# Kernel optimization log

Hardware: AMD Instinct MI355X
Metric: run time of the kernel (lower is better)

## Reference

```python
import jax, jax.numpy as jnp
import numpy as np

COULOMB_CONSTANT = 14.399645351950548  # eV * Angstrom
ENERGY_SCALE = 1.0
NOISE = 1e-8  # numerical_noise added to pairwise distances
B, N, D, U, E = 64, 512, 128, 64, 7


def tanhshrink(x):
    return x - jnp.tanh(x)


def chi_mlp(h, W1, b1, W2, b2, W3, b3):
    # MLP(dims=[D, U, U, 1], activation=Tanhshrink, activate_last=True)
    h = tanhshrink(h @ W1 + b1)
    h = tanhshrink(h @ W2 + b2)
    h = tanhshrink(h @ W3 + b3)
    return h  # [..., 1]


def setup_inputs() -> dict:
    key = jax.random.key(0)
    ks = jax.random.split(key, 8)
    return {
        "pos": jax.random.normal(ks[0], (B, N, 3), dtype=jnp.float32) * 3.0,
        "node_feats": jax.random.normal(ks[1], (B, N, D), dtype=jnp.float32),
        "node_type": jax.random.randint(ks[2], (B, N), 0, E),
        "total_charge": jax.random.normal(ks[3], (B,), dtype=jnp.float32),
        "hardness": jnp.ones((E,), dtype=jnp.float32),   # hardness_readout Parameter
        "sigma": jnp.ones((E,), dtype=jnp.float32),      # sigma Parameter (is_sigma_train)
        "W1": jax.random.normal(ks[4], (D, U), dtype=jnp.float32) / np.float32(np.sqrt(D)),
        "b1": jnp.zeros((U,), dtype=jnp.float32),
        "W2": jax.random.normal(ks[5], (U, U), dtype=jnp.float32) / np.float32(np.sqrt(U)),
        "b2": jnp.zeros((U,), dtype=jnp.float32),
        "W3": jax.random.normal(ks[6], (U, 1), dtype=jnp.float32) / np.float32(np.sqrt(U)),
        "b3": jnp.zeros((1,), dtype=jnp.float32),
    }


def reference(pos, node_feats, node_type, total_charge, hardness, sigma,
              W1, b1, W2, b2, W3, b3):
    k = jnp.float32(COULOMB_CONSTANT / ENERGY_SCALE)
    chi = chi_mlp(node_feats, W1, b1, W2, b2, W3, b3)[..., 0]          # [B, N]
    hard = hardness[node_type]                                          # [B, N]
    sig = sigma[node_type]                                              # [B, N]

    # Pairwise distances (per graph, dense O(N^2))
    diff = pos[:, :, None, :] - pos[:, None, :, :]                      # [B, N, N, 3]
    bond_dist = jnp.sqrt(jnp.sum(diff * diff, axis=-1)) + NOISE         # [B, N, N]
    gamma_ij = jnp.sqrt(sig[:, :, None] ** 2 + sig[:, None, :] ** 2)    # [B, N, N]

    a = k * jax.lax.erf(bond_dist / (jnp.sqrt(jnp.float32(2.0)) * gamma_ij)) / bond_dist

    # Diagonal self term: hardness_i + k / (sqrt(pi) * gamma_ii), gamma_ii = sqrt(2)*sigma_i
    gamma_ii = jnp.sqrt(jnp.float32(2.0)) * sig                         # [B, N]
    diag = hard + k / (jnp.sqrt(jnp.float32(np.pi)) * gamma_ii)         # [B, N]
    idx = jnp.arange(N)
    A = a.at[:, idx, idx].add(diag)                                     # [B, N, N]

    # Bordered system enforcing total charge constraint
    Bm = jnp.ones((B, N + 1, N + 1), dtype=pos.dtype)
    Bm = Bm.at[:, :N, :N].set(A)
    Bm = Bm.at[:, N, N].set(0.0)
    rhs = jnp.concatenate([-chi, total_charge[:, None]], axis=1)        # [B, N+1]

    x = jnp.linalg.solve(Bm, rhs[..., None])[..., 0]                    # [B, N+1]
    charges = x[:, :N]
    return charges, A
```

## Files before the change

kernel.cpp:

```cpp
#include <hip/hip_runtime.h>
#include <math.h>

constexpr int BB = 64, NN = 512, DD = 128, UU = 64;
constexpr float KCOUL = 14.399645351950548f;
constexpr float NOISEF = 1e-8f;
#define M_PIF 3.14159265358979323846f

typedef __attribute__((ext_vector_type(8))) short bfrag;
typedef __attribute__((ext_vector_type(4))) float ffrag;

__device__ __forceinline__ unsigned short f2bf(float f) {
  unsigned int u = __float_as_uint(f);
  u += 0x7fffu + ((u >> 16) & 1u);
  return (unsigned short)(u >> 16);
}
__device__ __forceinline__ float bf2f(unsigned short h) {
  return __uint_as_float((unsigned int)h << 16);
}
__device__ __forceinline__ float fast_erf(float x) {
  float t2 = x * x;
  float small_v = 1.1283791671f * x *
      fmaf(t2, fmaf(t2, fmaf(t2, fmaf(t2, 4.6296296e-3f, -2.3809524e-2f),
                             0.1f), -0.33333333f), 1.0f);
  float t = __builtin_amdgcn_rcpf(fmaf(0.3275911f, x, 1.0f));
  float p = fmaf(fmaf(fmaf(fmaf(1.061405429f, t, -1.453152027f),
                           t, 1.421413741f), t, -0.284496736f), t, 0.254829592f);
  float big_v = fmaf(-p * t, __expf(-t2), 1.0f);
  return x < 0.5f ? small_v : big_v;
}
__device__ __forceinline__ float fast_tanh(float x) {
  float ax = fabsf(x);
  float e = __expf(2.0f * ax);
  float t = 1.0f - 2.0f * __builtin_amdgcn_rcpf(e + 1.0f);
  return __builtin_copysignf(t, x);
}

__global__ __launch_bounds__(256) void chi_kernel(
    const float* __restrict__ feats, const float* __restrict__ W1,
    const float* __restrict__ b1, const float* __restrict__ W2,
    const float* __restrict__ b2, const float* __restrict__ W3,
    const float* __restrict__ b3, float* __restrict__ chi)
{
  int wave = threadIdx.x >> 6, lane = threadIdx.x & 63;
  int row0 = __builtin_amdgcn_readfirstlane((blockIdx.x * 4 + wave) * 4);
  const float* f = feats + (size_t)row0 * DD;
  __shared__ float sh[4][4][UU];

  float a0 = b1[lane], a1 = a0, a2 = a0, a3 = a0;
  #pragma unroll 8
  for (int d = 0; d < DD; ++d) {
    float wv = W1[d * UU + lane];
    a0 = fmaf(f[d],          wv, a0);
    a1 = fmaf(f[DD + d],     wv, a1);
    a2 = fmaf(f[2 * DD + d], wv, a2);
    a3 = fmaf(f[3 * DD + d], wv, a3);
  }
  sh[wave][0][lane] = a0 - fast_tanh(a0);
  sh[wave][1][lane] = a1 - fast_tanh(a1);
  sh[wave][2][lane] = a2 - fast_tanh(a2);
  sh[wave][3][lane] = a3 - fast_tanh(a3);
  __builtin_amdgcn_s_waitcnt(0);
  float c0 = b2[lane], c1 = c0, c2 = c0, c3 = c0;
  #pragma unroll 8
  for (int u = 0; u < UU; ++u) {
    float wv = W2[u * UU + lane];
    c0 = fmaf(sh[wave][0][u], wv, c0);
    c1 = fmaf(sh[wave][1][u], wv, c1);
    c2 = fmaf(sh[wave][2][u], wv, c2);
    c3 = fmaf(sh[wave][3][u], wv, c3);
  }
  float w3 = W3[lane];
  float p0 = (c0 - fast_tanh(c0)) * w3;
  float p1 = (c1 - fast_tanh(c1)) * w3;
  float p2 = (c2 - fast_tanh(c2)) * w3;
  float p3 = (c3 - fast_tanh(c3)) * w3;
  #pragma unroll
  for (int off = 32; off; off >>= 1) {
    p0 += __shfl_down(p0, off, 64);
    p1 += __shfl_down(p1, off, 64);
    p2 += __shfl_down(p2, off, 64);
    p3 += __shfl_down(p3, off, 64);
  }
  if (lane == 0) {
    float bb = b3[0];
    float z0 = p0 + bb, z1 = p1 + bb, z2v = p2 + bb, z3 = p3 + bb;
    chi[row0]     = z0 - fast_tanh(z0);
    chi[row0 + 1] = z1 - fast_tanh(z1);
    chi[row0 + 2] = z2v - fast_tanh(z2v);
    chi[row0 + 3] = z3 - fast_tanh(z3);
  }
}

__global__ __launch_bounds__(256) void build_A_kernel(
    const float* __restrict__ pos, const int* __restrict__ ntype,
    const float* __restrict__ hardness, const float* __restrict__ sigma,
    float* __restrict__ Aout, unsigned short* __restrict__ Abf)
{
  int b = blockIdx.y;
  int r0 = blockIdx.x * 16;
  __shared__ float px[NN], py[NN], pz[NN], s2[NN], hd[NN];
  __shared__ unsigned short tile[16 * NN];
  for (int n = threadIdx.x; n < NN; n += 256) {
    const float* p = pos + ((size_t)b * NN + n) * 3;
    px[n] = p[0]; py[n] = p[1]; pz[n] = p[2];
    int ty = ntype[b * NN + n];
    float s = sigma[ty];
    s2[n] = s * s;
    hd[n] = hardness[ty];
  }
  __syncthreads();
  int c0 = (threadIdx.x & 127) << 2;
  int rsub = threadIdx.x >> 7;
  float* outB = Aout + (size_t)b * NN * NN;
  for (int k = 0; k < 8; ++k) {
    int i = r0 + (k << 1) + rsub;
    float pxi = px[i], pyi = py[i], pzi = pz[i], s2i = s2[i];
    float4 v;
    float* vp = &v.x;
    #pragma unroll
    for (int c = 0; c < 4; ++c) {
      int j = c0 + c;
      float dx = pxi - px[j], dy = pyi - py[j], dz = pzi - pz[j];
      float d = sqrtf(fmaf(dx, dx, fmaf(dy, dy, dz * dz))) + NOISEF;
      float arg = d * __builtin_amdgcn_rsqf(2.0f * (s2i + s2[j]));
      float val = KCOUL * fast_erf(arg) * __builtin_amdgcn_rcpf(d);
      if (j == i) val += hd[i] + KCOUL * __builtin_amdgcn_rsqf(2.0f * M_PIF * s2i);
      vp[c] = val;
    }
    *reinterpret_cast<float4*>(outB + (size_t)i * NN + c0) = v;
    if (Abf) {
      ushort4 wv;
      wv.x = f2bf(v.x); wv.y = f2bf(v.y); wv.z = f2bf(v.z); wv.w = f2bf(v.w);
      int loc = ((c0 >> 5) << 9) + (((c0 >> 3) & 3) << 7) + ((i & 15) << 3) + (c0 & 7);
      *reinterpret_cast<ushort4*>(tile + loc) = wv;
    }
  }
  if (Abf) {
    __syncthreads();
    const uint4* src = reinterpret_cast<const uint4*>(tile);
    uint4* dst = reinterpret_cast<uint4*>(Abf + (size_t)b * NN * NN +
                                          ((size_t)(r0 >> 4) << 13));
    #pragma unroll
    for (int k = 0; k < 4; ++k)
      dst[threadIdx.x + k * 256] = src[threadIdx.x + k * 256];
  }
}

__device__ __forceinline__ float4 blockReduce4(float4 v, float4* wred, int t) {
  #pragma unroll
  for (int off = 32; off; off >>= 1) {
    v.x += __shfl_down(v.x, off, 64);
    v.y += __shfl_down(v.y, off, 64);
    v.z += __shfl_down(v.z, off, 64);
    v.w += __shfl_down(v.w, off, 64);
  }
  __syncthreads();
  if ((t & 63) == 0) wred[t >> 6] = v;
  __syncthreads();
  float4 r = wred[0];
  #pragma unroll
  for (int k = 1; k < 16; ++k) {
    float4 u = wred[k];
    r.x += u.x; r.y += u.y; r.z += u.z; r.w += u.w;
  }
  return r;
}

__global__ __launch_bounds__(1024) void cg_kernel_bf(
    const unsigned short* __restrict__ Abf, const float* __restrict__ tq,
    float* __restrict__ qout )
{
  int b = blockIdx.x;
  const unsigned short* A = Abf + (size_t)b * NN * NN;
  int t = threadIdx.x;
  int lane = t & 63, w = t >> 6;
  constexpr int PAD = NN + 32;
  __shared__ float2 p01[NN], q01[NN], r01[NN], x01[NN], w01[NN];
  __shared__ __align__(16) unsigned short rsplit[4 * PAD];
  __shared__ float4 wred[16];

  float2 z2 = make_float2(0.f, 0.f);
  float2 rsq = z2;
  if (t < NN) {
    float c = qout[b * NN + t];
    float2 rv = make_float2(-c, 1.0f);
    r01[t] = rv; x01[t] = z2; p01[t] = z2; q01[t] = z2;
    unsigned short h0 = f2bf(rv.x), h1 = f2bf(rv.y);
    rsplit[t] = h0;            rsplit[PAD + t] = h1;
    rsplit[2 * PAD + t] = f2bf(rv.x - bf2f(h0));
    rsplit[3 * PAD + t] = f2bf(rv.y - bf2f(h1));
    rsq = make_float2(rv.x * rv.x, rv.y * rv.y);
  }
  float4 rr0 = blockReduce4(make_float4(rsq.x, rsq.y, 0.f, 0.f), wred, t);
  float tol0 = fmaxf(1e-4f * rr0.x, 1e-12f);
  float tol1 = fmaxf(1e-4f * rr0.y, 1e-12f);
  bool act0 = rr0.x > tol0, act1 = rr0.y > tol1;

  const int m  = lane & 15;
  const int qd = lane >> 4;
  const unsigned short* aw0 = A + ((size_t)(2 * w) << 13) + lane * 8;
  const unsigned short* aw1 = aw0 + 8192;
  const unsigned short* bhi = rsplit + (m & 1) * PAD;
  const unsigned short* blo = rsplit + 2 * PAD + (m & 1) * PAD;

  float muold0 = 1.f, muold1 = 1.f, alold0 = 1.f, alold1 = 1.f;
  for (int k = 0; k < 24 && (act0 || act1); ++k) {
    ffrag acc0 = {0.f, 0.f, 0.f, 0.f};
    ffrag acc1 = {0.f, 0.f, 0.f, 0.f};
    #pragma unroll 4
    for (int c = 0; c < 16; ++c) {
      int bo = c * 32 + qd * 8;
      bfrag bh = *reinterpret_cast<const bfrag*>(bhi + bo);
      bfrag bl = *reinterpret_cast<const bfrag*>(blo + bo);
      bfrag a0 = *reinterpret_cast<const bfrag*>(aw0 + c * 512);
      bfrag a1 = *reinterpret_cast<const bfrag*>(aw1 + c * 512);
      acc0 = __builtin_amdgcn_mfma_f32_16x16x32_bf16(a0, bh, acc0, 0, 0, 0);
      acc0 = __builtin_amdgcn_mfma_f32_16x16x32_bf16(a0, bl, acc0, 0, 0, 0);
      acc1 = __builtin_amdgcn_mfma_f32_16x16x32_bf16(a1, bh, acc1, 0, 0, 0);
      acc1 = __builtin_amdgcn_mfma_f32_16x16x32_bf16(a1, bl, acc1, 0, 0, 0);
    }
    if (m < 2) {
      int rbase = qd * 4;
      #pragma unroll
      for (int r = 0; r < 4; ++r) {
        reinterpret_cast<float*>(&w01[w * 32 + rbase + r])[m]      = acc0[r];
        reinterpret_cast<float*>(&w01[w * 32 + 16 + rbase + r])[m] = acc1[r];
      }
    }
    __syncthreads();

    float4 dp = make_float4(0.f, 0.f, 0.f, 0.f);
    if (t < NN) {
      float2 rv = r01[t], wv = w01[t];
      dp = make_float4(rv.x * rv.x, rv.x * wv.x, rv.y * rv.y, rv.y * wv.y);
    }
    float4 s = blockReduce4(dp, wred, t);
    if (act0 && s.x <= tol0) act0 = false;
    if (act1 && s.z <= tol1) act1 = false;
    if (!act0 && !act1) break;
    float be0 = 0.f, al0 = 0.f, be1 = 0.f, al1 = 0.f;
    if (act0) {
      be0 = k ? s.x / muold0 : 0.f;
      al0 = s.x / (s.y - be0 * s.x / alold0);
      muold0 = s.x; alold0 = al0;
    }
    if (act1) {
      be1 = k ? s.z / muold1 : 0.f;
      al1 = s.z / (s.w - be1 * s.z / alold1);
      muold1 = s.z; alold1 = al1;
    }

    if (t < NN) {
      float2 rv = r01[t], wv = w01[t], pv = p01[t], qv = q01[t], xv = x01[t];
      if (act0) {
        pv.x = fmaf(be0, pv.x, rv.x);
        qv.x = fmaf(be0, qv.x, wv.x);
        xv.x = fmaf(al0, pv.x, xv.x);
        rv.x = fmaf(-al0, qv.x, rv.x);
      }
      if (act1) {
        pv.y = fmaf(be1, pv.y, rv.y);
        qv.y = fmaf(be1, qv.y, wv.y);
        xv.y = fmaf(al1, pv.y, xv.y);
        rv.y = fmaf(-al1, qv.y, rv.y);
      }
      p01[t] = pv; q01[t] = qv; x01[t] = xv; r01[t] = rv;
      unsigned short h0 = f2bf(rv.x), h1 = f2bf(rv.y);
      rsplit[t] = h0;            rsplit[PAD + t] = h1;
      rsplit[2 * PAD + t] = f2bf(rv.x - bf2f(h0));
      rsplit[3 * PAD + t] = f2bf(rv.y - bf2f(h1));
    }
    __syncthreads();
  }

  float2 sv = z2;
  if (t < NN) sv = x01[t];
  float4 s = blockReduce4(make_float4(sv.x, sv.y, 0.f, 0.f), wred, t);
  float lam = (s.x - tq[b]) / s.y;
  if (t < NN) qout[b * NN + t] = x01[t].x - lam * x01[t].y;
}

__device__ __forceinline__ float2 blockReduce2(float2 v, float2* wred, int t) {
  #pragma unroll
  for (int off = 32; off; off >>= 1) {
    v.x += __shfl_down(v.x, off, 64);
    v.y += __shfl_down(v.y, off, 64);
  }
  __syncthreads();
  if ((t & 63) == 0) wred[t >> 6] = v;
  __syncthreads();
  float2 r = wred[0];
  #pragma unroll
  for (int k = 1; k < 16; ++k) { r.x += wred[k].x; r.y += wred[k].y; }
  return r;
}

__global__ __launch_bounds__(1024) void cg_kernel_f32(
    const float* __restrict__ Aall, const float* __restrict__ tq,
    float* __restrict__ qout)
{
  int b = blockIdx.x;
  const float* A = Aall + (size_t)b * NN * NN;
  int t = threadIdx.x;
  __shared__ float2 p01[NN], q01[NN], r01[NN], x01[NN];
  __shared__ float4 sacc0[8][128];
  __shared__ float4 sacc1[8][128];
  __shared__ float2 wred[16];

  float2 z2 = make_float2(0.f, 0.f);
  float2 rsq = z2;
  if (t < NN) {
    float b0 = -qout[b * NN + t];
    x01[t] = z2;
    r01[t] = make_float2(b0, 1.0f);
    p01[t] = make_float2(b0, 1.0f);
    rsq = make_float2(b0 * b0, 1.0f);
  }
  float2 rr = blockReduce2(rsq, wred, t);
  float tol0 = fmaxf(1e-4f * rr.x, 1e-12f);
  float tol1 = fmaxf(1e-4f * rr.y, 1e-12f);
  const int c4 = (t & 127) << 2;
  const int jr = t >> 7;
  for (int it = 0; it < 24; ++it) {
    bool act0 = rr.x > tol0, act1 = rr.y > tol1;
    if (!act0 && !act1) break;
    {
      const float* ap = A + (size_t)(jr * 64) * NN + c4;
      float4 a0 = make_float4(0.f, 0.f, 0.f, 0.f);
      float4 a1 = a0;
      #pragma unroll 8
      for (int mI = 0; mI < 64; ++mI) {
        float4 av = *reinterpret_cast<const float4*>(ap);
        ap += NN;
        float2 pj = p01[jr * 64 + mI];
        a0.x = fmaf(av.x, pj.x, a0.x); a0.y = fmaf(av.y, pj.x, a0.y);
        a0.z = fmaf(av.z, pj.x, a0.z); a0.w = fmaf(av.w, pj.x, a0.w);
        a1.x = fmaf(av.x, pj.y, a1.x); a1.y = fmaf(av.y, pj.y, a1.y);
        a1.z = fmaf(av.z, pj.y, a1.z); a1.w = fmaf(av.w, pj.y, a1.w);
      }
      sacc0[jr][t & 127] = a0;
      sacc1[jr][t & 127] = a1;
    }
    __syncthreads();
    float2 dv = z2;
    if (t < NN) {
      const float* f0 = reinterpret_cast<const float*>(sacc0);
      const float* f1 = reinterpret_cast<const float*>(sacc1);
      float s0 = 0.f, s1 = 0.f;
      #pragma unroll
      for (int g = 0; g < 8; ++g) { s0 += f0[g * 512 + t]; s1 += f1[g * 512 + t]; }
      q01[t] = make_float2(s0, s1);
      float2 pv = p01[t];
      dv.x = s0 * pv.x; dv.y = s1 * pv.y;
    }
    float2 pq = blockReduce2(dv, wred, t);
    float al0 = act0 ? rr.x / pq.x : 0.f;
    float al1 = act1 ? rr.y / pq.y : 0.f;
    float2 rn = z2;
    if (t < NN) {
      float2 xv = x01[t], rv = r01[t], pv = p01[t], qv = q01[t];
      xv.x = fmaf(al0, pv.x, xv.x);  xv.y = fmaf(al1, pv.y, xv.y);
      rv.x = fmaf(-al0, qv.x, rv.x); rv.y = fmaf(-al1, qv.y, rv.y);
      x01[t] = xv; r01[t] = rv;
      rn.x = rv.x * rv.x; rn.y = rv.y * rv.y;
    }
    float2 rrn = blockReduce2(rn, wred, t);
    float be0 = act0 ? rrn.x / rr.x : 0.f;
    float be1 = act1 ? rrn.y / rr.y : 0.f;
    if (t < NN) {
      float2 rv = r01[t], pv = p01[t];
      pv.x = fmaf(be0, pv.x, rv.x);
      pv.y = fmaf(be1, pv.y, rv.y);
      p01[t] = pv;
    }
    rr = rrn;
    __syncthreads();
  }
  float2 sv = z2;
  if (t < NN) sv = x01[t];
  float2 s = blockReduce2(sv, wred, t);
  float lam = (s.x - tq[b]) / s.y;
  if (t < NN) qout[b * NN + t] = x01[t].x - lam * x01[t].y;
}

extern "C" void kernel_launch(void* const* d_in, const int* in_sizes, int n_in,
                              void* d_out, int out_size, void* d_ws, size_t ws_size,
                              hipStream_t stream) {
  const float* pos      = (const float*)d_in[0];
  const float* feats    = (const float*)d_in[1];
  const int*   ntype    = (const int*)  d_in[2];
  const float* tq       = (const float*)d_in[3];
  const float* hardness = (const float*)d_in[4];
  const float* sigma    = (const float*)d_in[5];
  const float* W1 = (const float*)d_in[6];
  const float* b1 = (const float*)d_in[7];
  const float* W2 = (const float*)d_in[8];
  const float* b2 = (const float*)d_in[9];
  const float* W3 = (const float*)d_in[10];
  const float* b3 = (const float*)d_in[11];

  float* out  = (float*)d_out;
  float* chi  = out;
  float* Aout = out + BB * NN;

  const size_t bf_bytes = (size_t)BB * NN * NN * sizeof(unsigned short);
  const bool use_bf = ws_size >= bf_bytes;
  unsigned short* Abf = use_bf ? (unsigned short*)d_ws : nullptr;

  chi_kernel<<<dim3(BB * NN / 16), dim3(256), 0, stream>>>(feats, W1, b1, W2, b2, W3, b3, chi);
  build_A_kernel<<<dim3(NN / 16, BB), dim3(256), 0, stream>>>(pos, ntype, hardness, sigma, Aout, Abf);
  if (use_bf)
    cg_kernel_bf<<<dim3(BB), dim3(1024), 0, stream>>>(Abf, tq, chi);
  else
    cg_kernel_f32<<<dim3(BB), dim3(1024), 0, stream>>>(Aout, tq, chi);
}
```

Before: 255.0 us.

## Keep CG vectors in registers and halve per-iteration block barriers

The CG solver kernel now maps all 1024 threads to a (row, right-hand-side) pair and keeps the p, q, x and r vectors in registers instead of shared-memory float2 arrays. Dot products use wave shuffles with stride 2 to separate the two right-hand sides, then a single shared-memory partial-sum exchange. This cuts each iteration from four barriers to two and removes the LDS traffic for the vector updates. The risk is correctness around same-wave reads of w01 without a barrier, which rely on in-order LDS access within a wave.

```diff
diff --git a/kernel.cpp b/kernel.cpp
--- a/kernel.cpp
+++ b/kernel.cpp
@@ -146,26 +146,6 @@
   }
 }
 
-__device__ __forceinline__ float4 blockReduce4(float4 v, float4* wred, int t) {
-  #pragma unroll
-  for (int off = 32; off; off >>= 1) {
-    v.x += __shfl_down(v.x, off, 64);
-    v.y += __shfl_down(v.y, off, 64);
-    v.z += __shfl_down(v.z, off, 64);
-    v.w += __shfl_down(v.w, off, 64);
-  }
-  __syncthreads();
-  if ((t & 63) == 0) wred[t >> 6] = v;
-  __syncthreads();
-  float4 r = wred[0];
-  #pragma unroll
-  for (int k = 1; k < 16; ++k) {
-    float4 u = wred[k];
-    r.x += u.x; r.y += u.y; r.z += u.z; r.w += u.w;
-  }
-  return r;
-}
-
 __global__ __launch_bounds__(1024) void cg_kernel_bf(
     const unsigned short* __restrict__ Abf, const float* __restrict__ tq,
     float* __restrict__ qout )
@@ -175,33 +155,38 @@
   int t = threadIdx.x;
   int lane = t & 63, w = t >> 6;
   constexpr int PAD = NN + 32;
-  __shared__ float2 p01[NN], q01[NN], r01[NN], x01[NN], w01[NN];
   __shared__ __align__(16) unsigned short rsplit[4 * PAD];
+  __shared__ float w01[2 * NN];
   __shared__ float4 wred[16];
 
-  float2 z2 = make_float2(0.f, 0.f);
-  float2 rsq = z2;
-  if (t < NN) {
-    float c = qout[b * NN + t];
-    float2 rv = make_float2(-c, 1.0f);
-    r01[t] = rv; x01[t] = z2; p01[t] = z2; q01[t] = z2;
-    unsigned short h0 = f2bf(rv.x), h1 = f2bf(rv.y);
-    rsplit[t] = h0;            rsplit[PAD + t] = h1;
-    rsplit[2 * PAD + t] = f2bf(rv.x - bf2f(h0));
-    rsplit[3 * PAD + t] = f2bf(rv.y - bf2f(h1));
-    rsq = make_float2(rv.x * rv.x, rv.y * rv.y);
-  }
-  float4 rr0 = blockReduce4(make_float4(rsq.x, rsq.y, 0.f, 0.f), wred, t);
-  float tol0 = fmaxf(1e-4f * rr0.x, 1e-12f);
-  float tol1 = fmaxf(1e-4f * rr0.y, 1e-12f);
-  bool act0 = rr0.x > tol0, act1 = rr0.y > tol1;
-
+  const int row = w * 32 + (lane >> 1);
+  const int rhs = lane & 1;
   const int m  = lane & 15;
   const int qd = lane >> 4;
   const unsigned short* aw0 = A + ((size_t)(2 * w) << 13) + lane * 8;
   const unsigned short* aw1 = aw0 + 8192;
   const unsigned short* bhi = rsplit + (m & 1) * PAD;
   const unsigned short* blo = rsplit + 2 * PAD + (m & 1) * PAD;
+
+  float rv = rhs ? 1.0f : -qout[b * NN + row];
+  float xv = 0.f, pv = 0.f, qv = 0.f;
+  {
+    unsigned short h = f2bf(rv);
+    rsplit[rhs * PAD + row] = h;
+    rsplit[2 * PAD + rhs * PAD + row] = f2bf(rv - bf2f(h));
+  }
+  float rr = rv * rv;
+  #pragma unroll
+  for (int off = 2; off < 64; off <<= 1) rr += __shfl_down(rr, off, 64);
+  if (lane < 2) reinterpret_cast<float2*>(&wred[w])[lane] = make_float2(rr, 0.f);
+  __syncthreads();
+  float mu0 = 0.f, mu1 = 0.f;
+  #pragma unroll
+  for (int g = 0; g < 16; ++g) { mu0 += wred[g].x; mu1 += wred[g].z; }
+  float tol0 = fmaxf(1e-4f * mu0, 1e-12f);
+  float tol1 = fmaxf(1e-4f * mu1, 1e-12f);
+  bool act0 = mu0 > tol0, act1 = mu1 > tol1;
+  __syncthreads();
 
   float muold0 = 1.f, muold1 = 1.f, alold0 = 1.f, alold1 = 1.f;
   for (int k = 0; k < 24 && (act0 || act1); ++k) {
@@ -223,61 +208,66 @@
       int rbase = qd * 4;
       #pragma unroll
       for (int r = 0; r < 4; ++r) {
-        reinterpret_cast<float*>(&w01[w * 32 + rbase + r])[m]      = acc0[r];
-        reinterpret_cast<float*>(&w01[w * 32 + 16 + rbase + r])[m] = acc1[r];
+        w01[(w * 32 + rbase + r) * 2 + m]      = acc0[r];
+        w01[(w * 32 + 16 + rbase + r) * 2 + m] = acc1[r];
       }
     }
+    float wv = w01[row * 2 + rhs];
+
+    float pr = rv * rv, pw = rv * wv;
+    #pragma unroll
+    for (int off = 2; off < 64; off <<= 1) {
+      pr += __shfl_down(pr, off, 64);
+      pw += __shfl_down(pw, off, 64);
+    }
+    if (lane < 2) reinterpret_cast<float2*>(&wred[w])[lane] = make_float2(pr, pw);
     __syncthreads();
 
-    float4 dp = make_float4(0.f, 0.f, 0.f, 0.f);
-    if (t < NN) {
-      float2 rv = r01[t], wv = w01[t];
-      dp = make_float4(rv.x * rv.x, rv.x * wv.x, rv.y * rv.y, rv.y * wv.y);
-    }
-    float4 s = blockReduce4(dp, wred, t);
-    if (act0 && s.x <= tol0) act0 = false;
-    if (act1 && s.z <= tol1) act1 = false;
+    float s0 = 0.f, n0 = 0.f, s1 = 0.f, n1 = 0.f;
+    #pragma unroll
+    for (int g = 0; g < 16; ++g) {
+      float4 u = wred[g];
+      s0 += u.x; n0 += u.y; s1 += u.z; n1 += u.w;
+    }
+    if (act0 && s0 <= tol0) act0 = false;
+    if (act1 && s1 <= tol1) act1 = false;
     if (!act0 && !act1) break;
     float be0 = 0.f, al0 = 0.f, be1 = 0.f, al1 = 0.f;
     if (act0) {
-      be0 = k ? s.x / muold0 : 0.f;
-      al0 = s.x / (s.y - be0 * s.x / alold0);
-      muold0 = s.x; alold0 = al0;
+      be0 = k ? s0 / muold0 : 0.f;
+      al0 = s0 / (n0 - be0 * s0 / alold0);
+      muold0 = s0; alold0 = al0;
     }
     if (act1) {
-      be1 = k ? s.z / muold1 : 0.f;
-      al1 = s.z / (s.w - be1 * s.z / alold1);
-      muold1 = s.z; alold1 = al1;
-    }
-
-    if (t < NN) {
-      float2 rv = r01[t], wv = w01[t], pv = p01[t], qv = q01[t], xv = x01[t];
-      if (act0) {
-        pv.x = fmaf(be0, pv.x, rv.x);
-        qv.x = fmaf(be0, qv.x, wv.x);
-        xv.x = fmaf(al0, pv.x, xv.x);
-        rv.x = fmaf(-al0, qv.x, rv.x);
-      }
-      if (act1) {
-        pv.y = fmaf(be1, pv.y, rv.y);
-        qv.y = fmaf(be1, qv.y, wv.y);
-        xv.y = fmaf(al1, pv.y, xv.y);
-        rv.y = fmaf(-al1, qv.y, rv.y);
-      }
-      p01[t] = pv; q01[t] = qv; x01[t] = xv; r01[t] = rv;
-      unsigned short h0 = f2bf(rv.x), h1 = f2bf(rv.y);
-      rsplit[t] = h0;            rsplit[PAD + t] = h1;
-      rsplit[2 * PAD + t] = f2bf(rv.x - bf2f(h0));
-      rsplit[3 * PAD + t] = f2bf(rv.y - bf2f(h1));
-    }
+      be1 = k ? s1 / muold1 : 0.f;
+      al1 = s1 / (n1 - be1 * s1 / alold1);
+      muold1 = s1; alold1 = al1;
+    }
+    float be = rhs ? be1 : be0;
+    float al = rhs ? al1 : al0;
+
+    pv = fmaf(be, pv, rv);
+    qv = fmaf(be, qv, wv);
+    xv = fmaf(al, pv, xv);
+    rv = fmaf(-al, qv, rv);
+    unsigned short h = f2bf(rv);
+    rsplit[rhs * PAD + row] = h;
+    rsplit[2 * PAD + rhs * PAD + row] = f2bf(rv - bf2f(h));
     __syncthreads();
   }
 
-  float2 sv = z2;
-  if (t < NN) sv = x01[t];
-  float4 s = blockReduce4(make_float4(sv.x, sv.y, 0.f, 0.f), wred, t);
-  float lam = (s.x - tq[b]) / s.y;
-  if (t < NN) qout[b * NN + t] = x01[t].x - lam * x01[t].y;
+  __syncthreads();
+  float sx = xv;
+  #pragma unroll
+  for (int off = 2; off < 64; off <<= 1) sx += __shfl_down(sx, off, 64);
+  if (lane < 2) reinterpret_cast<float2*>(&wred[w])[lane] = make_float2(sx, 0.f);
+  __syncthreads();
+  float sum0 = 0.f, sum1 = 0.f;
+  #pragma unroll
+  for (int g = 0; g < 16; ++g) { sum0 += wred[g].x; sum1 += wred[g].z; }
+  float lam = (sum0 - tq[b]) / sum1;
+  float xpart = __shfl_xor(xv, 1, 64);
+  if (rhs == 0) qout[b * NN + row] = xv - lam * xpart;
 }
 
 __device__ __forceinline__ float2 blockReduce2(float2 v, float2* wred, int t) {
```

Result: faster. 249.1 us (-2.3%).
